# Kernel optimization log

Measured on AMD Instinct MI355X. Metric: run time of the kernel, lower is better.

The kernel has to match this reference:

```python
import jax, jax.numpy as jnp
import numpy as np


def setup_inputs() -> dict:
    key = jax.random.key(0)
    k1, k2 = jax.random.split(key)
    pred = jax.random.normal(k1, (1, 2048, 512), dtype=jnp.float32)
    cand = jax.random.normal(k2, (1, 65536, 512), dtype=jnp.float32)
    return {
        "predicted_transaction_company": pred,
        "future_transaction_companies_inc_current_data": cand,
    }


def reference(predicted_transaction_company, future_transaction_companies_inc_current_data):
    # torch.cdist with p=2 on [1,P,D] x [1,R,D] -> [1,P,R]; squeeze(0) -> [P,R]; global min.
    x = predicted_transaction_company[0]                       # [P, D]
    y = future_transaction_companies_inc_current_data[0]       # [R, D]
    sq = (
        jnp.sum(x * x, axis=-1)[:, None]
        + jnp.sum(y * y, axis=-1)[None, :]
        - 2.0 * jnp.einsum("pd,rd->pr", x, y)
    )                                                          # [P, R]
    distances = jnp.sqrt(jnp.maximum(sq, 0.0))
    return jnp.min(distances)
```

## Files before the change

### kernel.cpp

```cpp
#include <hip/hip_runtime.h>
#include <stdint.h>

#define P 2048
#define R 65536
#define DD 512
#define BM 256
#define BN 256
#define BK 64
#define NT (DD / BK)

typedef __attribute__((ext_vector_type(8))) short short8;
typedef __attribute__((ext_vector_type(4))) float f32x4;

__device__ inline unsigned short f2bf(float f) {
  unsigned int u = __float_as_uint(f);
  u += 0x7fffu + ((u >> 16) & 1u);
  return (unsigned short)(u >> 16);
}

__device__ inline void gload_lds16(const void* g, void* l) {
  __builtin_amdgcn_global_load_lds(
      (const __attribute__((address_space(1))) unsigned int*)g,
      (__attribute__((address_space(3))) unsigned int*)l,
      16, 0, 0);
}

__global__ __launch_bounds__(256) void k_convert(
    const float* __restrict__ pred, const float* __restrict__ cand,
    unsigned short* __restrict__ Abf, unsigned short* __restrict__ Bbf,
    float* __restrict__ nx, float* __restrict__ ny,
    unsigned int* __restrict__ minp)
{
  if (blockIdx.x == 0 && threadIdx.x == 0) *minp = 0x7f800000u;
  int gw   = (blockIdx.x * 256 + threadIdx.x) >> 6;
  int lane = threadIdx.x & 63;
  if (gw >= P + R) return;
  const float* src; unsigned short* dst; float* np;
  if (gw < P) { src = pred + (size_t)gw * DD; dst = Abf + (size_t)gw * DD; np = nx + gw; }
  else { int r = gw - P; src = cand + (size_t)r * DD; dst = Bbf + (size_t)r * DD; np = ny + r; }
  const float4* s4 = ((const float4*)src) + lane * 2;
  float4 v0 = s4[0], v1 = s4[1];
  float ss = v0.x*v0.x + v0.y*v0.y + v0.z*v0.z + v0.w*v0.w
           + v1.x*v1.x + v1.y*v1.y + v1.z*v1.z + v1.w*v1.w;
  union { unsigned short h[8]; uint4 v; } pk;
  pk.h[0]=f2bf(v0.x); pk.h[1]=f2bf(v0.y); pk.h[2]=f2bf(v0.z); pk.h[3]=f2bf(v0.w);
  pk.h[4]=f2bf(v1.x); pk.h[5]=f2bf(v1.y); pk.h[6]=f2bf(v1.z); pk.h[7]=f2bf(v1.w);
  *(uint4*)(dst + (size_t)lane * 8) = pk.v;
  #pragma unroll
  for (int off = 32; off; off >>= 1) ss += __shfl_down(ss, off, 64);
  if (lane == 0) *np = ss;
}

__global__ __launch_bounds__(512, 2) void k_gemm_min(
    const unsigned short* __restrict__ Abf, const unsigned short* __restrict__ Bbf,
    const float* __restrict__ nx, const float* __restrict__ ny,
    unsigned int* __restrict__ minp)
{
  __shared__ __align__(16) unsigned short As[2][BM * BK];
  __shared__ __align__(16) unsigned short Bs[2][BN * BK];
  __shared__ float wmin[8];

  const int tid  = threadIdx.x;
  const int wave = tid >> 6;
  const int lane = tid & 63;

  const int raw = blockIdx.x;
  const int wg  = (raw & 7) * 256 + (raw >> 3);
  const int by  = wg & 7;
  const int bx  = wg >> 3;
  const int rowA0 = by * BM, rowB0 = bx * BN;
  const int wr = wave >> 2;
  const int wc = wave & 3;

  f32x4 zero = {0.f, 0.f, 0.f, 0.f};
  f32x4 acc[8][4];
  #pragma unroll
  for (int i = 0; i < 8; ++i)
    #pragma unroll
    for (int j = 0; j < 4; ++j) acc[i][j] = zero;

  const int rloc = lane >> 3;
  const int cswz = (lane & 7) ^ rloc;
  const unsigned short* gA[4]; const unsigned short* gB[4];
  int lOff[4];
  #pragma unroll
  for (int t = 0; t < 4; ++t) {
    const int ii = wave * 4 + t;
    const int rr = ii * 8 + rloc;
    gA[t] = Abf + (size_t)(rowA0 + rr) * DD + cswz * 8;
    gB[t] = Bbf + (size_t)(rowB0 + rr) * DD + cswz * 8;
    lOff[t] = ii * 512;
  }

#define STAGE(c, kt) do { const int _k0 = (kt) * BK;            \
    _Pragma("unroll")                                           \
    for (int _t = 0; _t < 4; ++_t) {                            \
      gload_lds16(gA[_t] + _k0, &As[(c)][lOff[_t]]);            \
      gload_lds16(gB[_t] + _k0, &Bs[(c)][lOff[_t]]);            \
    } } while (0)

  const int m = lane & 15, quad = lane >> 4, mb = m & 7;
  const int aRow0 = (wr * 128 + m) * BK;
  const int bRow0 = (wc * 64  + m) * BK;
  const int swz0 = ((quad    ) ^ mb) * 8;
  const int swz1 = ((quad + 4) ^ mb) * 8;

  STAGE(0, 0);
  STAGE(1, 1);
  asm volatile("s_waitcnt vmcnt(8)" ::: "memory");
  __builtin_amdgcn_s_barrier();

  for (int kt = 0; kt < NT; ++kt) {
    const int c = kt & 1;
    const unsigned short* A0 = &As[c][0];
    const unsigned short* B0 = &Bs[c][0];

    short8 bfr[4][2];
    #pragma unroll
    for (int j = 0; j < 4; ++j) {
      const unsigned short* bp = B0 + bRow0 + j * 16 * BK;
      bfr[j][0] = *(const short8*)(bp + swz0);
      bfr[j][1] = *(const short8*)(bp + swz1);
    }
    #pragma unroll
    for (int mh = 0; mh < 2; ++mh) {
      short8 af[4][2];
      #pragma unroll
      for (int i = 0; i < 4; ++i) {
        const unsigned short* ap = A0 + aRow0 + (mh * 4 + i) * 16 * BK;
        af[i][0] = *(const short8*)(ap + swz0);
        af[i][1] = *(const short8*)(ap + swz1);
      }
      __builtin_amdgcn_s_setprio(1);
      #pragma unroll
      for (int i = 0; i < 4; ++i)
        #pragma unroll
        for (int j = 0; j < 4; ++j) {
          acc[mh*4+i][j] = __builtin_amdgcn_mfma_f32_16x16x32_bf16(af[i][0], bfr[j][0], acc[mh*4+i][j], 0, 0, 0);
          acc[mh*4+i][j] = __builtin_amdgcn_mfma_f32_16x16x32_bf16(af[i][1], bfr[j][1], acc[mh*4+i][j], 0, 0, 0);
        }
      __builtin_amdgcn_s_setprio(0);
      asm volatile("" ::: "memory");
    }

    if (kt < NT - 1) {
      __builtin_amdgcn_s_barrier();
      if (kt + 2 < NT) {
        STAGE(c, kt + 2);
        asm volatile("s_waitcnt vmcnt(8)" ::: "memory");
      } else {
        asm volatile("s_waitcnt vmcnt(0)" ::: "memory");
      }
      __builtin_amdgcn_s_barrier();
    }
  }
#undef STAGE

  float lmin = 3.4e38f;
  #pragma unroll
  for (int i = 0; i < 8; ++i) {
    const int mbase = rowA0 + wr * 128 + i * 16 + quad * 4;
    float4 nxv = *(const float4*)(nx + mbase);
    #pragma unroll
    for (int j = 0; j < 4; ++j) {
      const int n = rowB0 + wc * 64 + j * 16 + m;
      const float nyv = ny[n];
      f32x4 a = acc[i][j];
      lmin = fminf(lmin, nxv.x + nyv - 2.0f * a[0]);
      lmin = fminf(lmin, nxv.y + nyv - 2.0f * a[1]);
      lmin = fminf(lmin, nxv.z + nyv - 2.0f * a[2]);
      lmin = fminf(lmin, nxv.w + nyv - 2.0f * a[3]);
    }
  }
  #pragma unroll
  for (int off = 32; off; off >>= 1) lmin = fminf(lmin, __shfl_down(lmin, off, 64));
  if (lane == 0) wmin[wave] = lmin;
  __syncthreads();
  if (tid == 0) {
    float mn = wmin[0];
    #pragma unroll
    for (int w = 1; w < 8; ++w) mn = fminf(mn, wmin[w]);
    atomicMin(minp, __float_as_uint(fmaxf(mn, 0.0f)));
  }
}

__global__ __launch_bounds__(64) void k_initmin(unsigned int* minp) {
  if (threadIdx.x == 0) *minp = 0x7f800000u;
}

__global__ __launch_bounds__(256) void k_brute(
    const float* __restrict__ pred, const float* __restrict__ cand,
    unsigned int* __restrict__ minp)
{
  __shared__ float yrow[DD];
  __shared__ float wm[4];
  const int c = blockIdx.x;
  for (int i = threadIdx.x; i < DD; i += 256) yrow[i] = cand[(size_t)c * DD + i];
  __syncthreads();
  float lmin = 3.4e38f;
  for (int p = threadIdx.x; p < P; p += 256) {
    const float* xp = pred + (size_t)p * DD;
    float s = 0.f;
    for (int k = 0; k < DD; ++k) { float d = xp[k] - yrow[k]; s = fmaf(d, d, s); }
    lmin = fminf(lmin, s);
  }
  #pragma unroll
  for (int off = 32; off; off >>= 1) lmin = fminf(lmin, __shfl_down(lmin, off, 64));
  if ((threadIdx.x & 63) == 0) wm[threadIdx.x >> 6] = lmin;
  __syncthreads();
  if (threadIdx.x == 0) {
    float mn = fminf(fminf(wm[0], wm[1]), fminf(wm[2], wm[3]));
    atomicMin(minp, __float_as_uint(fmaxf(mn, 0.0f)));
  }
}

__global__ __launch_bounds__(64) void k_finalize(const unsigned int* minp, float* out) {
  if (threadIdx.x == 0) out[0] = sqrtf(__uint_as_float(*minp));
}

extern "C" void kernel_launch(void* const* d_in, const int* in_sizes, int n_in,
                              void* d_out, int out_size, void* d_ws, size_t ws_size,
                              hipStream_t stream) {
  const float* pred = (const float*)d_in[0];
  const float* cand = (const float*)d_in[1];
  float* out = (float*)d_out;

  unsigned int* minp = (unsigned int*)d_ws;
  float* wsf = (float*)d_ws;
  float* nx = wsf + 16;
  float* ny = nx + P;
  unsigned short* Abf = (unsigned short*)(ny + R);
  unsigned short* Bbf = Abf + (size_t)P * DD;
  const size_t need = (size_t)(16 + P + R) * 4 + ((size_t)P * DD + (size_t)R * DD) * 2;

  if (ws_size >= need) {
    const int rows = P + R;
    k_convert<<<rows / 4, 256, 0, stream>>>(pred, cand, Abf, Bbf, nx, ny, minp);
    k_gemm_min<<<(P / BM) * (R / BN), 512, 0, stream>>>(Abf, Bbf, nx, ny, minp);
  } else {
    k_initmin<<<1, 64, 0, stream>>>(minp);
    k_brute<<<R, 256, 0, stream>>>(pred, cand, minp);
  }
  k_finalize<<<1, 64, 0, stream>>>(minp, out);
}
```

Before: 340.0 us.

## Split GEMM k-step into four quadrant phases interleaving loads with MFMA

Restructures the main GEMM loop into four sub-phases, one per A/B quadrant. Each phase issues a slice of the next tiles' global-to-LDS loads and then runs its MFMA block, with barriers and sched_barriers around each phase. The aim is to spread memory traffic across the compute stream instead of bursting all loads after the full tile compute, and to keep fewer fragments live at once. It adds more barriers per iteration and relies on fragile vmcnt counts and partial-buffer reuse ordering.

```diff
diff --git a/kernel.cpp b/kernel.cpp
--- a/kernel.cpp
+++ b/kernel.cpp
@@ -81,23 +81,28 @@
 
   const int rloc = lane >> 3;
   const int cswz = (lane & 7) ^ rloc;
-  const unsigned short* gA[4]; const unsigned short* gB[4];
-  int lOff[4];
-  #pragma unroll
-  for (int t = 0; t < 4; ++t) {
-    const int ii = wave * 4 + t;
-    const int rr = ii * 8 + rloc;
-    gA[t] = Abf + (size_t)(rowA0 + rr) * DD + cswz * 8;
-    gB[t] = Bbf + (size_t)(rowB0 + rr) * DD + cswz * 8;
-    lOff[t] = ii * 512;
-  }
-
-#define STAGE(c, kt) do { const int _k0 = (kt) * BK;            \
-    _Pragma("unroll")                                           \
-    for (int _t = 0; _t < 4; ++_t) {                            \
-      gload_lds16(gA[_t] + _k0, &As[(c)][lOff[_t]]);            \
-      gload_lds16(gB[_t] + _k0, &Bs[(c)][lOff[_t]]);            \
-    } } while (0)
+  const unsigned short* aBase = Abf + (size_t)(rowA0 + rloc) * DD + cswz * 8;
+  const unsigned short* bBase = Bbf + (size_t)(rowB0 + rloc) * DD + cswz * 8;
+  const int ldsLane = lane * 8;
+  int gA[2][2], gB[2][2];
+  #pragma unroll
+  for (int t = 0; t < 2; ++t) {
+    const int idx = wave * 2 + t;
+    #pragma unroll
+    for (int h = 0; h < 2; ++h) {
+      gA[h][t] = ((idx >> 3) << 4) | (h << 3) | (idx & 7);
+      gB[h][t] = ((idx >> 2) << 3) | (h << 2) | (idx & 3);
+    }
+  }
+
+#define STAGE_A(h, s, tt) do { _Pragma("unroll")                              \
+    for (int _t = 0; _t < 2; ++_t) { const int _g = gA[h][_t];                \
+      gload_lds16(aBase + (size_t)_g * (8 * DD) + (tt) * BK,                  \
+                  &As[s][_g * 512 + ldsLane]); } } while (0)
+#define STAGE_B(h, s, tt) do { _Pragma("unroll")                              \
+    for (int _t = 0; _t < 2; ++_t) { const int _g = gB[h][_t];                \
+      gload_lds16(bBase + (size_t)_g * (8 * DD) + (tt) * BK,                  \
+                  &Bs[s][_g * 512 + ldsLane]); } } while (0)
 
   const int m = lane & 15, quad = lane >> 4, mb = m & 7;
   const int aRow0 = (wr * 128 + m) * BK;
@@ -105,56 +110,106 @@
   const int swz0 = ((quad    ) ^ mb) * 8;
   const int swz1 = ((quad + 4) ^ mb) * 8;
 
-  STAGE(0, 0);
-  STAGE(1, 1);
-  asm volatile("s_waitcnt vmcnt(8)" ::: "memory");
+  STAGE_A(0, 0, 0); STAGE_B(0, 0, 0); STAGE_B(1, 0, 0); STAGE_A(1, 0, 0);
+  STAGE_A(0, 1, 1); STAGE_B(0, 1, 1); STAGE_B(1, 1, 1);
+  asm volatile("s_waitcnt vmcnt(6)" ::: "memory");
   __builtin_amdgcn_s_barrier();
 
-  for (int kt = 0; kt < NT; ++kt) {
-    const int c = kt & 1;
-    const unsigned short* A0 = &As[c][0];
-    const unsigned short* B0 = &Bs[c][0];
-
-    short8 bfr[4][2];
-    #pragma unroll
-    for (int j = 0; j < 4; ++j) {
+  #pragma unroll 1
+  for (int T = 0; T < NT; ++T) {
+    const int s = T & 1;
+    const unsigned short* A0 = &As[s][0];
+    const unsigned short* B0 = &Bs[s][0];
+    short8 af[4][2], bfr[4][2];
+
+    #pragma unroll
+    for (int i = 0; i < 4; ++i) {
+      const unsigned short* ap = A0 + aRow0 + i * 16 * BK;
+      af[i][0] = *(const short8*)(ap + swz0);
+      af[i][1] = *(const short8*)(ap + swz1);
+    }
+    #pragma unroll
+    for (int j = 0; j < 2; ++j) {
       const unsigned short* bp = B0 + bRow0 + j * 16 * BK;
       bfr[j][0] = *(const short8*)(bp + swz0);
       bfr[j][1] = *(const short8*)(bp + swz1);
     }
-    #pragma unroll
-    for (int mh = 0; mh < 2; ++mh) {
-      short8 af[4][2];
+    if (T + 1 < NT) STAGE_A(1, (T + 1) & 1, T + 1);
+    __builtin_amdgcn_s_barrier();
+    asm volatile("s_waitcnt lgkmcnt(0)" ::: "memory");
+    __builtin_amdgcn_sched_barrier(0);
+    __builtin_amdgcn_s_setprio(1);
+    #pragma unroll
+    for (int i = 0; i < 4; ++i)
       #pragma unroll
-      for (int i = 0; i < 4; ++i) {
-        const unsigned short* ap = A0 + aRow0 + (mh * 4 + i) * 16 * BK;
-        af[i][0] = *(const short8*)(ap + swz0);
-        af[i][1] = *(const short8*)(ap + swz1);
+      for (int j = 0; j < 2; ++j) {
+        acc[i][j] = __builtin_amdgcn_mfma_f32_16x16x32_bf16(af[i][0], bfr[j][0], acc[i][j], 0, 0, 0);
+        acc[i][j] = __builtin_amdgcn_mfma_f32_16x16x32_bf16(af[i][1], bfr[j][1], acc[i][j], 0, 0, 0);
       }
-      __builtin_amdgcn_s_setprio(1);
+    __builtin_amdgcn_s_setprio(0);
+    __builtin_amdgcn_s_barrier();
+
+    #pragma unroll
+    for (int j = 2; j < 4; ++j) {
+      const unsigned short* bp = B0 + bRow0 + j * 16 * BK;
+      bfr[j][0] = *(const short8*)(bp + swz0);
+      bfr[j][1] = *(const short8*)(bp + swz1);
+    }
+    if (T + 2 < NT) STAGE_A(0, s, T + 2);
+    __builtin_amdgcn_s_barrier();
+    asm volatile("s_waitcnt lgkmcnt(0)" ::: "memory");
+    __builtin_amdgcn_sched_barrier(0);
+    __builtin_amdgcn_s_setprio(1);
+    #pragma unroll
+    for (int i = 0; i < 4; ++i)
       #pragma unroll
-      for (int i = 0; i < 4; ++i)
-        #pragma unroll
-        for (int j = 0; j < 4; ++j) {
-          acc[mh*4+i][j] = __builtin_amdgcn_mfma_f32_16x16x32_bf16(af[i][0], bfr[j][0], acc[mh*4+i][j], 0, 0, 0);
-          acc[mh*4+i][j] = __builtin_amdgcn_mfma_f32_16x16x32_bf16(af[i][1], bfr[j][1], acc[mh*4+i][j], 0, 0, 0);
-        }
-      __builtin_amdgcn_s_setprio(0);
-      asm volatile("" ::: "memory");
-    }
-
-    if (kt < NT - 1) {
-      __builtin_amdgcn_s_barrier();
-      if (kt + 2 < NT) {
-        STAGE(c, kt + 2);
-        asm volatile("s_waitcnt vmcnt(8)" ::: "memory");
-      } else {
-        asm volatile("s_waitcnt vmcnt(0)" ::: "memory");
+      for (int j = 2; j < 4; ++j) {
+        acc[i][j] = __builtin_amdgcn_mfma_f32_16x16x32_bf16(af[i][0], bfr[j][0], acc[i][j], 0, 0, 0);
+        acc[i][j] = __builtin_amdgcn_mfma_f32_16x16x32_bf16(af[i][1], bfr[j][1], acc[i][j], 0, 0, 0);
       }
-      __builtin_amdgcn_s_barrier();
-    }
-  }
-#undef STAGE
+    __builtin_amdgcn_s_setprio(0);
+    __builtin_amdgcn_s_barrier();
+
+    #pragma unroll
+    for (int i = 0; i < 4; ++i) {
+      const unsigned short* ap = A0 + aRow0 + (4 + i) * 16 * BK;
+      af[i][0] = *(const short8*)(ap + swz0);
+      af[i][1] = *(const short8*)(ap + swz1);
+    }
+    if (T + 2 < NT) STAGE_B(0, s, T + 2);
+    __builtin_amdgcn_s_barrier();
+    asm volatile("s_waitcnt lgkmcnt(0)" ::: "memory");
+    __builtin_amdgcn_sched_barrier(0);
+    __builtin_amdgcn_s_setprio(1);
+    #pragma unroll
+    for (int i = 0; i < 4; ++i)
+      #pragma unroll
+      for (int j = 0; j < 2; ++j) {
+        acc[4 + i][j] = __builtin_amdgcn_mfma_f32_16x16x32_bf16(af[i][0], bfr[j][0], acc[4 + i][j], 0, 0, 0);
+        acc[4 + i][j] = __builtin_amdgcn_mfma_f32_16x16x32_bf16(af[i][1], bfr[j][1], acc[4 + i][j], 0, 0, 0);
+      }
+    __builtin_amdgcn_s_setprio(0);
+    __builtin_amdgcn_s_barrier();
+
+    if (T + 2 < NT) STAGE_B(1, s, T + 2);
+    __builtin_amdgcn_s_barrier();
+    __builtin_amdgcn_s_setprio(1);
+    #pragma unroll
+    for (int i = 0; i < 4; ++i)
+      #pragma unroll
+      for (int j = 2; j < 4; ++j) {
+        acc[4 + i][j] = __builtin_amdgcn_mfma_f32_16x16x32_bf16(af[i][0], bfr[j][0], acc[4 + i][j], 0, 0, 0);
+        acc[4 + i][j] = __builtin_amdgcn_mfma_f32_16x16x32_bf16(af[i][1], bfr[j][1], acc[4 + i][j], 0, 0, 0);
+      }
+    __builtin_amdgcn_s_setprio(0);
+    if (T < NT - 1) {
+      if (T + 1 == NT - 1) { asm volatile("s_waitcnt vmcnt(0)" ::: "memory"); }
+      else                 { asm volatile("s_waitcnt vmcnt(6)" ::: "memory"); }
+    }
+    __builtin_amdgcn_s_barrier();
+  }
+#undef STAGE_A
+#undef STAGE_B
 
   float lmin = 3.4e38f;
   #pragma unroll
```

Measured after the change: 336.3 us. Within noise of the previous version (-1.1%).

## Restructure GEMM k-loop pipeline with split LDS waits; grid-stride convert kernel

Applied to the files above, without the earlier changes.

The GEMM main loop is reorganised. It now issues the next tile's global-to-LDS load at the top of each iteration and uses one barrier pair per iteration instead of the previous post-compute double barrier. LDS fragment reads are split so MFMAs on the first B half can start after a partial lgkmcnt wait, which overlaps LDS latency with matrix math. The convert kernel becomes a grid-stride loop over a fixed 2048 blocks to reduce launch and tail overhead. The change risks different register pressure, and the prefetch is now issued only one tile ahead rather than two.

```diff
diff --git a/kernel.cpp b/kernel.cpp
--- a/kernel.cpp
+++ b/kernel.cpp
@@ -32,23 +32,25 @@
     unsigned int* __restrict__ minp)
 {
   if (blockIdx.x == 0 && threadIdx.x == 0) *minp = 0x7f800000u;
-  int gw   = (blockIdx.x * 256 + threadIdx.x) >> 6;
-  int lane = threadIdx.x & 63;
-  if (gw >= P + R) return;
-  const float* src; unsigned short* dst; float* np;
-  if (gw < P) { src = pred + (size_t)gw * DD; dst = Abf + (size_t)gw * DD; np = nx + gw; }
-  else { int r = gw - P; src = cand + (size_t)r * DD; dst = Bbf + (size_t)r * DD; np = ny + r; }
-  const float4* s4 = ((const float4*)src) + lane * 2;
-  float4 v0 = s4[0], v1 = s4[1];
-  float ss = v0.x*v0.x + v0.y*v0.y + v0.z*v0.z + v0.w*v0.w
-           + v1.x*v1.x + v1.y*v1.y + v1.z*v1.z + v1.w*v1.w;
-  union { unsigned short h[8]; uint4 v; } pk;
-  pk.h[0]=f2bf(v0.x); pk.h[1]=f2bf(v0.y); pk.h[2]=f2bf(v0.z); pk.h[3]=f2bf(v0.w);
-  pk.h[4]=f2bf(v1.x); pk.h[5]=f2bf(v1.y); pk.h[6]=f2bf(v1.z); pk.h[7]=f2bf(v1.w);
-  *(uint4*)(dst + (size_t)lane * 8) = pk.v;
-  #pragma unroll
-  for (int off = 32; off; off >>= 1) ss += __shfl_down(ss, off, 64);
-  if (lane == 0) *np = ss;
+  const int lane = threadIdx.x & 63;
+  const int wv   = (blockIdx.x << 2) | (threadIdx.x >> 6);
+  const int nw   = gridDim.x << 2;
+  for (int gw = wv; gw < P + R; gw += nw) {
+    const float* src; unsigned short* dst; float* np;
+    if (gw < P) { src = pred + (size_t)gw * DD; dst = Abf + (size_t)gw * DD; np = nx + gw; }
+    else { int r = gw - P; src = cand + (size_t)r * DD; dst = Bbf + (size_t)r * DD; np = ny + r; }
+    const float4* s4 = ((const float4*)src) + lane * 2;
+    float4 v0 = s4[0], v1 = s4[1];
+    float ss = v0.x*v0.x + v0.y*v0.y + v0.z*v0.z + v0.w*v0.w
+             + v1.x*v1.x + v1.y*v1.y + v1.z*v1.z + v1.w*v1.w;
+    union { unsigned short h[8]; uint4 v; } pk;
+    pk.h[0]=f2bf(v0.x); pk.h[1]=f2bf(v0.y); pk.h[2]=f2bf(v0.z); pk.h[3]=f2bf(v0.w);
+    pk.h[4]=f2bf(v1.x); pk.h[5]=f2bf(v1.y); pk.h[6]=f2bf(v1.z); pk.h[7]=f2bf(v1.w);
+    *(uint4*)(dst + (size_t)lane * 8) = pk.v;
+    #pragma unroll
+    for (int off = 32; off; off >>= 1) ss += __shfl_down(ss, off, 64);
+    if (lane == 0) *np = ss;
+  }
 }
 
 __global__ __launch_bounds__(512, 2) void k_gemm_min(
@@ -82,21 +84,20 @@
   const int rloc = lane >> 3;
   const int cswz = (lane & 7) ^ rloc;
   const unsigned short* gA[4]; const unsigned short* gB[4];
-  int lOff[4];
+  int lofs[4];
   #pragma unroll
   for (int t = 0; t < 4; ++t) {
     const int ii = wave * 4 + t;
-    const int rr = ii * 8 + rloc;
-    gA[t] = Abf + (size_t)(rowA0 + rr) * DD + cswz * 8;
-    gB[t] = Bbf + (size_t)(rowB0 + rr) * DD + cswz * 8;
-    lOff[t] = ii * 512;
-  }
-
-#define STAGE(c, kt) do { const int _k0 = (kt) * BK;            \
+    gA[t] = Abf + (size_t)(rowA0 + ii * 8 + rloc) * DD + cswz * 8;
+    gB[t] = Bbf + (size_t)(rowB0 + ii * 8 + rloc) * DD + cswz * 8;
+    lofs[t] = ii * 512;
+  }
+
+#define STAGE(s, kt) do { const int _k0 = (kt) * BK;            \
     _Pragma("unroll")                                           \
     for (int _t = 0; _t < 4; ++_t) {                            \
-      gload_lds16(gA[_t] + _k0, &As[(c)][lOff[_t]]);            \
-      gload_lds16(gB[_t] + _k0, &Bs[(c)][lOff[_t]]);            \
+      gload_lds16(gA[_t] + _k0, &As[s][lofs[_t]]);              \
+      gload_lds16(gB[_t] + _k0, &Bs[s][lofs[_t]]);              \
     } } while (0)
 
   const int m = lane & 15, quad = lane >> 4, mb = m & 7;
@@ -106,53 +107,88 @@
   const int swz1 = ((quad + 4) ^ mb) * 8;
 
   STAGE(0, 0);
-  STAGE(1, 1);
-  asm volatile("s_waitcnt vmcnt(8)" ::: "memory");
-  __builtin_amdgcn_s_barrier();
-
-  for (int kt = 0; kt < NT; ++kt) {
-    const int c = kt & 1;
-    const unsigned short* A0 = &As[c][0];
-    const unsigned short* B0 = &Bs[c][0];
-
-    short8 bfr[4][2];
-    #pragma unroll
-    for (int j = 0; j < 4; ++j) {
+
+  #pragma unroll 2
+  for (int T = 0; T < NT; ++T) {
+    const int s = T & 1;
+    if (T + 1 < NT) {
+      STAGE(s ^ 1, T + 1);
+      asm volatile("s_waitcnt vmcnt(8)" ::: "memory");
+    } else {
+      asm volatile("s_waitcnt vmcnt(0)" ::: "memory");
+    }
+    __builtin_amdgcn_s_barrier();
+    __builtin_amdgcn_sched_barrier(0);
+
+    const unsigned short* A0 = &As[s][0];
+    const unsigned short* B0 = &Bs[s][0];
+    short8 af[4][2], b0[2][2], b1[2][2];
+
+    #pragma unroll
+    for (int i = 0; i < 4; ++i) {
+      const unsigned short* ap = A0 + aRow0 + i * 16 * BK;
+      af[i][0] = *(const short8*)(ap + swz0);
+      af[i][1] = *(const short8*)(ap + swz1);
+    }
+    #pragma unroll
+    for (int j = 0; j < 2; ++j) {
       const unsigned short* bp = B0 + bRow0 + j * 16 * BK;
-      bfr[j][0] = *(const short8*)(bp + swz0);
-      bfr[j][1] = *(const short8*)(bp + swz1);
-    }
-    #pragma unroll
-    for (int mh = 0; mh < 2; ++mh) {
-      short8 af[4][2];
-      #pragma unroll
-      for (int i = 0; i < 4; ++i) {
-        const unsigned short* ap = A0 + aRow0 + (mh * 4 + i) * 16 * BK;
-        af[i][0] = *(const short8*)(ap + swz0);
-        af[i][1] = *(const short8*)(ap + swz1);
-      }
-      __builtin_amdgcn_s_setprio(1);
-      #pragma unroll
-      for (int i = 0; i < 4; ++i)
-        #pragma unroll
-        for (int j = 0; j < 4; ++j) {
-          acc[mh*4+i][j] = __builtin_amdgcn_mfma_f32_16x16x32_bf16(af[i][0], bfr[j][0], acc[mh*4+i][j], 0, 0, 0);
-          acc[mh*4+i][j] = __builtin_amdgcn_mfma_f32_16x16x32_bf16(af[i][1], bfr[j][1], acc[mh*4+i][j], 0, 0, 0);
-        }
-      __builtin_amdgcn_s_setprio(0);
-      asm volatile("" ::: "memory");
-    }
-
-    if (kt < NT - 1) {
-      __builtin_amdgcn_s_barrier();
-      if (kt + 2 < NT) {
-        STAGE(c, kt + 2);
-        asm volatile("s_waitcnt vmcnt(8)" ::: "memory");
-      } else {
-        asm volatile("s_waitcnt vmcnt(0)" ::: "memory");
-      }
-      __builtin_amdgcn_s_barrier();
-    }
+      b0[j][0] = *(const short8*)(bp + swz0);
+      b0[j][1] = *(const short8*)(bp + swz1);
+    }
+    #pragma unroll
+    for (int j = 0; j < 2; ++j) {
+      const unsigned short* bp = B0 + bRow0 + (2 + j) * 16 * BK;
+      b1[j][0] = *(const short8*)(bp + swz0);
+      b1[j][1] = *(const short8*)(bp + swz1);
+    }
+    asm volatile("s_waitcnt lgkmcnt(4)" ::: "memory");
+    __builtin_amdgcn_sched_barrier(0);
+    __builtin_amdgcn_s_setprio(1);
+    #pragma unroll
+    for (int i = 0; i < 4; ++i)
+      #pragma unroll
+      for (int j = 0; j < 2; ++j) {
+        acc[i][j] = __builtin_amdgcn_mfma_f32_16x16x32_bf16(af[i][0], b0[j][0], acc[i][j], 0, 0, 0);
+        acc[i][j] = __builtin_amdgcn_mfma_f32_16x16x32_bf16(af[i][1], b0[j][1], acc[i][j], 0, 0, 0);
+      }
+    __builtin_amdgcn_s_setprio(0);
+    asm volatile("s_waitcnt lgkmcnt(0)" ::: "memory");
+    __builtin_amdgcn_sched_barrier(0);
+    __builtin_amdgcn_s_setprio(1);
+    #pragma unroll
+    for (int i = 0; i < 4; ++i)
+      #pragma unroll
+      for (int j = 0; j < 2; ++j) {
+        acc[i][2 + j] = __builtin_amdgcn_mfma_f32_16x16x32_bf16(af[i][0], b1[j][0], acc[i][2 + j], 0, 0, 0);
+        acc[i][2 + j] = __builtin_amdgcn_mfma_f32_16x16x32_bf16(af[i][1], b1[j][1], acc[i][2 + j], 0, 0, 0);
+      }
+    __builtin_amdgcn_s_setprio(0);
+
+    #pragma unroll
+    for (int i = 0; i < 4; ++i) {
+      const unsigned short* ap = A0 + aRow0 + (4 + i) * 16 * BK;
+      af[i][0] = *(const short8*)(ap + swz0);
+      af[i][1] = *(const short8*)(ap + swz1);
+    }
+    asm volatile("s_waitcnt lgkmcnt(0)" ::: "memory");
+    __builtin_amdgcn_sched_barrier(0);
+    __builtin_amdgcn_s_setprio(1);
+    #pragma unroll
+    for (int i = 0; i < 4; ++i) {
+      #pragma unroll
+      for (int j = 0; j < 2; ++j) {
+        acc[4 + i][j]     = __builtin_amdgcn_mfma_f32_16x16x32_bf16(af[i][0], b0[j][0], acc[4 + i][j], 0, 0, 0);
+        acc[4 + i][j]     = __builtin_amdgcn_mfma_f32_16x16x32_bf16(af[i][1], b0[j][1], acc[4 + i][j], 0, 0, 0);
+      }
+      #pragma unroll
+      for (int j = 0; j < 2; ++j) {
+        acc[4 + i][2 + j] = __builtin_amdgcn_mfma_f32_16x16x32_bf16(af[i][0], b1[j][0], acc[4 + i][2 + j], 0, 0, 0);
+        acc[4 + i][2 + j] = __builtin_amdgcn_mfma_f32_16x16x32_bf16(af[i][1], b1[j][1], acc[4 + i][2 + j], 0, 0, 0);
+      }
+    }
+    __builtin_amdgcn_s_setprio(0);
+    __builtin_amdgcn_s_barrier();
   }
 #undef STAGE
 
@@ -234,8 +270,7 @@
   const size_t need = (size_t)(16 + P + R) * 4 + ((size_t)P * DD + (size_t)R * DD) * 2;
 
   if (ws_size >= need) {
-    const int rows = P + R;
-    k_convert<<<rows / 4, 256, 0, stream>>>(pred, cand, Abf, Bbf, nx, ny, minp);
+    k_convert<<<2048, 256, 0, stream>>>(pred, cand, Abf, Bbf, nx, ny, minp);
     k_gemm_min<<<(P / BM) * (R / BN), 512, 0, stream>>>(Abf, Bbf, nx, ny, minp);
   } else {
     k_initmin<<<1, 64, 0, stream>>>(minp);
```

Result: slower. 348.0 us (+2.3%).

## Pre-pack B into MFMA fragment layout and load B directly to registers

Applied to the files above, without the earlier changes.

The convert kernel now writes the candidate matrix in a layout that matches the MFMA B-fragment order, so each lane can fetch its B operands straight from global memory with contiguous 16-byte loads. B no longer goes through shared memory, which halves LDS usage and drops the B LDS reads. The main loop is restructured into an explicitly double-buffered register/LDS pipeline with sched barriers, and the convert kernel becomes grid-stride. The risks are higher register pressure from two B fragment buffers, and global-load latency sitting on the MFMA path, since B is reused from L2 rather than LDS across the tile.

```diff
diff --git a/kernel.cpp b/kernel.cpp
--- a/kernel.cpp
+++ b/kernel.cpp
@@ -27,37 +27,45 @@
 
 __global__ __launch_bounds__(256) void k_convert(
     const float* __restrict__ pred, const float* __restrict__ cand,
-    unsigned short* __restrict__ Abf, unsigned short* __restrict__ Bbf,
+    unsigned short* __restrict__ Abf, unsigned short* __restrict__ Bpk,
     float* __restrict__ nx, float* __restrict__ ny,
     unsigned int* __restrict__ minp)
 {
   if (blockIdx.x == 0 && threadIdx.x == 0) *minp = 0x7f800000u;
-  int gw   = (blockIdx.x * 256 + threadIdx.x) >> 6;
-  int lane = threadIdx.x & 63;
-  if (gw >= P + R) return;
-  const float* src; unsigned short* dst; float* np;
-  if (gw < P) { src = pred + (size_t)gw * DD; dst = Abf + (size_t)gw * DD; np = nx + gw; }
-  else { int r = gw - P; src = cand + (size_t)r * DD; dst = Bbf + (size_t)r * DD; np = ny + r; }
-  const float4* s4 = ((const float4*)src) + lane * 2;
-  float4 v0 = s4[0], v1 = s4[1];
-  float ss = v0.x*v0.x + v0.y*v0.y + v0.z*v0.z + v0.w*v0.w
-           + v1.x*v1.x + v1.y*v1.y + v1.z*v1.z + v1.w*v1.w;
-  union { unsigned short h[8]; uint4 v; } pk;
-  pk.h[0]=f2bf(v0.x); pk.h[1]=f2bf(v0.y); pk.h[2]=f2bf(v0.z); pk.h[3]=f2bf(v0.w);
-  pk.h[4]=f2bf(v1.x); pk.h[5]=f2bf(v1.y); pk.h[6]=f2bf(v1.z); pk.h[7]=f2bf(v1.w);
-  *(uint4*)(dst + (size_t)lane * 8) = pk.v;
-  #pragma unroll
-  for (int off = 32; off; off >>= 1) ss += __shfl_down(ss, off, 64);
-  if (lane == 0) *np = ss;
+  const int lane = threadIdx.x & 63;
+  const int wv   = (blockIdx.x << 2) | (threadIdx.x >> 6);
+  const int nw   = gridDim.x << 2;
+  for (int gw = wv; gw < P + R; gw += nw) {
+    const float* src; float* np;
+    if (gw < P) { src = pred + (size_t)gw * DD; np = nx + gw; }
+    else        { src = cand + (size_t)(gw - P) * DD; np = ny + (gw - P); }
+    const float4* s4 = ((const float4*)src) + lane * 2;
+    float4 v0 = s4[0], v1 = s4[1];
+    float ss = v0.x*v0.x + v0.y*v0.y + v0.z*v0.z + v0.w*v0.w
+             + v1.x*v1.x + v1.y*v1.y + v1.z*v1.z + v1.w*v1.w;
+    union { unsigned short h[8]; uint4 v; } pk;
+    pk.h[0]=f2bf(v0.x); pk.h[1]=f2bf(v0.y); pk.h[2]=f2bf(v0.z); pk.h[3]=f2bf(v0.w);
+    pk.h[4]=f2bf(v1.x); pk.h[5]=f2bf(v1.y); pk.h[6]=f2bf(v1.z); pk.h[7]=f2bf(v1.w);
+    if (gw < P) {
+      *(uint4*)(Abf + (size_t)gw * DD + lane * 8) = pk.v;
+    } else {
+      const int r = gw - P;
+      const size_t off = (((size_t)(r >> 6) * 16 + (lane >> 2)) * 4 + ((r >> 4) & 3)) * 512
+                       + (size_t)((lane & 3) * 16 + (r & 15)) * 8;
+      *(uint4*)(Bpk + off) = pk.v;
+    }
+    #pragma unroll
+    for (int off = 32; off; off >>= 1) ss += __shfl_down(ss, off, 64);
+    if (lane == 0) *np = ss;
+  }
 }
 
 __global__ __launch_bounds__(512, 2) void k_gemm_min(
-    const unsigned short* __restrict__ Abf, const unsigned short* __restrict__ Bbf,
+    const unsigned short* __restrict__ Abf, const unsigned short* __restrict__ Bpk,
     const float* __restrict__ nx, const float* __restrict__ ny,
     unsigned int* __restrict__ minp)
 {
   __shared__ __align__(16) unsigned short As[2][BM * BK];
-  __shared__ __align__(16) unsigned short Bs[2][BN * BK];
   __shared__ float wmin[8];
 
   const int tid  = threadIdx.x;
@@ -81,80 +89,87 @@
 
   const int rloc = lane >> 3;
   const int cswz = (lane & 7) ^ rloc;
-  const unsigned short* gA[4]; const unsigned short* gB[4];
-  int lOff[4];
+  const unsigned short* gA[4];
+  int lofs[4];
   #pragma unroll
   for (int t = 0; t < 4; ++t) {
     const int ii = wave * 4 + t;
-    const int rr = ii * 8 + rloc;
-    gA[t] = Abf + (size_t)(rowA0 + rr) * DD + cswz * 8;
-    gB[t] = Bbf + (size_t)(rowB0 + rr) * DD + cswz * 8;
-    lOff[t] = ii * 512;
-  }
-
-#define STAGE(c, kt) do { const int _k0 = (kt) * BK;            \
+    gA[t] = Abf + (size_t)(rowA0 + ii * 8 + rloc) * DD + cswz * 8;
+    lofs[t] = ii * 512;
+  }
+
+#define STAGE_A(s, kt) do { const int _k0 = (kt) * BK;          \
     _Pragma("unroll")                                           \
-    for (int _t = 0; _t < 4; ++_t) {                            \
-      gload_lds16(gA[_t] + _k0, &As[(c)][lOff[_t]]);            \
-      gload_lds16(gB[_t] + _k0, &Bs[(c)][lOff[_t]]);            \
-    } } while (0)
+    for (int _t = 0; _t < 4; ++_t)                              \
+      gload_lds16(gA[_t] + _k0, &As[s][lofs[_t]]);              \
+  } while (0)
+
+  const unsigned short* bbase = Bpk + (size_t)(bx * 4 + wc) * 64 * 512 + lane * 8;
+
+#define LOADB(dst, T) do {                                                    \
+    _Pragma("unroll")                                                         \
+    for (int _h = 0; _h < 2; ++_h)                                            \
+      _Pragma("unroll")                                                       \
+      for (int _j = 0; _j < 4; ++_j)                                          \
+        dst[_j][_h] = *(const short8*)(bbase +                                \
+            (size_t)((2 * (T) + _h) * 4 + _j) * 512);                         \
+  } while (0)
 
   const int m = lane & 15, quad = lane >> 4, mb = m & 7;
   const int aRow0 = (wr * 128 + m) * BK;
-  const int bRow0 = (wc * 64  + m) * BK;
-  const int swz0 = ((quad    ) ^ mb) * 8;
-  const int swz1 = ((quad + 4) ^ mb) * 8;
-
-  STAGE(0, 0);
-  STAGE(1, 1);
+  const int sw0 = ((quad    ) ^ mb) * 8;
+  const int sw1 = ((quad + 4) ^ mb) * 8;
+
+#define COMPUTE(s, bcur) do {                                                 \
+    _Pragma("unroll")                                                         \
+    for (int _mh = 0; _mh < 2; ++_mh)                                         \
+      _Pragma("unroll")                                                       \
+      for (int _h = 0; _h < 2; ++_h) {                                        \
+        short8 _af[4];                                                        \
+        const int _sw = _h ? sw1 : sw0;                                       \
+        _Pragma("unroll")                                                     \
+        for (int _i = 0; _i < 4; ++_i)                                        \
+          _af[_i] = *(const short8*)(&As[s][aRow0 + (_mh*4+_i)*16*BK + _sw]); \
+        __builtin_amdgcn_s_setprio(1);                                        \
+        _Pragma("unroll")                                                     \
+        for (int _i = 0; _i < 4; ++_i)                                        \
+          _Pragma("unroll")                                                   \
+          for (int _j = 0; _j < 4; ++_j)                                      \
+            acc[_mh*4+_i][_j] = __builtin_amdgcn_mfma_f32_16x16x32_bf16(      \
+                _af[_i], bcur[_j][_h], acc[_mh*4+_i][_j], 0, 0, 0);           \
+        __builtin_amdgcn_s_setprio(0);                                        \
+      }                                                                       \
+  } while (0)
+
+  short8 bA[4][2], bB[4][2];
+
+  STAGE_A(0, 0);
+  LOADB(bA, 0);
+  __builtin_amdgcn_sched_barrier(0);
   asm volatile("s_waitcnt vmcnt(8)" ::: "memory");
   __builtin_amdgcn_s_barrier();
 
-  for (int kt = 0; kt < NT; ++kt) {
-    const int c = kt & 1;
-    const unsigned short* A0 = &As[c][0];
-    const unsigned short* B0 = &Bs[c][0];
-
-    short8 bfr[4][2];
-    #pragma unroll
-    for (int j = 0; j < 4; ++j) {
-      const unsigned short* bp = B0 + bRow0 + j * 16 * BK;
-      bfr[j][0] = *(const short8*)(bp + swz0);
-      bfr[j][1] = *(const short8*)(bp + swz1);
-    }
-    #pragma unroll
-    for (int mh = 0; mh < 2; ++mh) {
-      short8 af[4][2];
-      #pragma unroll
-      for (int i = 0; i < 4; ++i) {
-        const unsigned short* ap = A0 + aRow0 + (mh * 4 + i) * 16 * BK;
-        af[i][0] = *(const short8*)(ap + swz0);
-        af[i][1] = *(const short8*)(ap + swz1);
-      }
-      __builtin_amdgcn_s_setprio(1);
-      #pragma unroll
-      for (int i = 0; i < 4; ++i)
-        #pragma unroll
-        for (int j = 0; j < 4; ++j) {
-          acc[mh*4+i][j] = __builtin_amdgcn_mfma_f32_16x16x32_bf16(af[i][0], bfr[j][0], acc[mh*4+i][j], 0, 0, 0);
-          acc[mh*4+i][j] = __builtin_amdgcn_mfma_f32_16x16x32_bf16(af[i][1], bfr[j][1], acc[mh*4+i][j], 0, 0, 0);
-        }
-      __builtin_amdgcn_s_setprio(0);
-      asm volatile("" ::: "memory");
-    }
-
-    if (kt < NT - 1) {
-      __builtin_amdgcn_s_barrier();
-      if (kt + 2 < NT) {
-        STAGE(c, kt + 2);
-        asm volatile("s_waitcnt vmcnt(8)" ::: "memory");
-      } else {
-        asm volatile("s_waitcnt vmcnt(0)" ::: "memory");
-      }
+  #pragma unroll 1
+  for (int T = 0; T < NT; T += 2) {
+    if (T + 1 < NT) { STAGE_A(1, T + 1); LOADB(bB, T + 1); }
+    __builtin_amdgcn_sched_barrier(0);
+    COMPUTE(0, bA);
+    __builtin_amdgcn_sched_barrier(0);
+    asm volatile("s_waitcnt vmcnt(8)" ::: "memory");
+    __builtin_amdgcn_s_barrier();
+
+    if (T + 1 < NT) {
+      if (T + 2 < NT) { STAGE_A(0, T + 2); LOADB(bA, T + 2); }
+      __builtin_amdgcn_sched_barrier(0);
+      COMPUTE(1, bB);
+      __builtin_amdgcn_sched_barrier(0);
+      asm volatile("s_waitcnt vmcnt(8)" ::: "memory");
       __builtin_amdgcn_s_barrier();
     }
   }
-#undef STAGE
+#undef STAGE_A
+#undef LOADB
+#undef COMPUTE
 
   float lmin = 3.4e38f;
   #pragma unroll
@@ -230,13 +245,12 @@
   float* nx = wsf + 16;
   float* ny = nx + P;
   unsigned short* Abf = (unsigned short*)(ny + R);
-  unsigned short* Bbf = Abf + (size_t)P * DD;
+  unsigned short* Bpk = Abf + (size_t)P * DD;
   const size_t need = (size_t)(16 + P + R) * 4 + ((size_t)P * DD + (size_t)R * DD) * 2;
 
   if (ws_size >= need) {
-    const int rows = P + R;
-    k_convert<<<rows / 4, 256, 0, stream>>>(pred, cand, Abf, Bbf, nx, ny, minp);
-    k_gemm_min<<<(P / BM) * (R / BN), 512, 0, stream>>>(Abf, Bbf, nx, ny, minp);
+    k_convert<<<2048, 256, 0, stream>>>(pred, cand, Abf, Bpk, nx, ny, minp);
+    k_gemm_min<<<(P / BM) * (R / BN), 512, 0, stream>>>(Abf, Bpk, nx, ny, minp);
   } else {
     k_initmin<<<1, 64, 0, stream>>>(minp);
     k_brute<<<R, 256, 0, stream>>>(pred, cand, minp);
```

Result: slower. 481.3 us (+41.5%).
